# Kernel optimization log

Hardware: AMD Instinct MI355X
Metric: run time of the kernel (lower is better)

The kernel has to match this reference:

```python
import jax, jax.numpy as jnp
import numpy as np

B_, L_, V = 256, 256, 44
DM, DI, DS, DR, NL = 256, 512, 16, 16, 6  # d_model, d_inner, d_state, dt_rank, n_layers
MLP_H = 128


def setup_inputs():
    key = jax.random.key(0)
    ks = jax.random.split(key, 16)
    def nrm(i, shape, s=0.02):
        return jax.random.normal(ks[i], shape, jnp.float32) * s
    tok = jax.random.randint(ks[0], (B_, L_), 0, V, dtype=jnp.int32)
    mask = jax.random.randint(ks[1], (B_, L_), 0, 2, dtype=jnp.int32)
    emb = nrm(2, (V, 64), 0.02)
    emb = emb.at[0].set(0.0)  # padding_idx=0
    conv_w = nrm(3, (DM, 64, 3), 0.05)
    bn_gamma = jnp.ones((DM,), jnp.float32)
    bn_beta = jnp.zeros((DM,), jnp.float32)
    in_proj_w = nrm(4, (NL, 2 * DI, DM))
    conv1d_w = nrm(5, (NL, DI, 4), 0.2)
    conv1d_b = jnp.zeros((NL, DI), jnp.float32)
    x_proj_w = nrm(6, (NL, DR + 2 * DS, DI))
    dt_proj_w = nrm(7, (NL, DI, DR), 0.1)
    dt_proj_b = -4.0 + nrm(8, (NL, DI), 0.5)
    A_log = jnp.log(jnp.arange(1, DS + 1, dtype=jnp.float32))[None, None, :] * jnp.ones((NL, DI, 1), jnp.float32)
    Dp = jnp.ones((NL, DI), jnp.float32)
    out_proj_w = nrm(9, (NL, DM, DI))
    norm1_w = jnp.ones((NL, DM), jnp.float32)
    norm2_w = jnp.ones((NL, DM), jnp.float32)
    fc1_w = nrm(10, (NL, 2 * MLP_H, DM))
    fc2_w = nrm(11, (NL, DM, MLP_H))
    normf_w = jnp.ones((DM,), jnp.float32)
    normf_b = jnp.zeros((DM,), jnp.float32)
    bind_w = nrm(12, (3, DM))
    bind_b = jnp.zeros((3,), jnp.float32)
    return {"smiles_token_id": tok, "smiles_token_mask": mask, "emb": emb, "conv_w": conv_w,
            "bn_gamma": bn_gamma, "bn_beta": bn_beta, "in_proj_w": in_proj_w, "conv1d_w": conv1d_w,
            "conv1d_b": conv1d_b, "x_proj_w": x_proj_w, "dt_proj_w": dt_proj_w, "dt_proj_b": dt_proj_b,
            "A_log": A_log, "Dp": Dp, "out_proj_w": out_proj_w, "norm1_w": norm1_w, "norm2_w": norm2_w,
            "fc1_w": fc1_w, "fc2_w": fc2_w, "normf_w": normf_w, "normf_b": normf_b,
            "bind_w": bind_w, "bind_b": bind_b}


def rmsnorm(x, w, eps=1e-4):
    return x * jax.lax.rsqrt(jnp.mean(x * x, -1, keepdims=True) + eps) * w


def layernorm(x, w, b, eps=1e-4):
    mu = jnp.mean(x, -1, keepdims=True)
    var = jnp.mean((x - mu) ** 2, -1, keepdims=True)
    return (x - mu) * jax.lax.rsqrt(var + eps) * w + b


def mamba1(x, inw, cw, cb, xpw, dtw, dtb, Alog, D, outw):
    # x: [B,L,DM]
    B, L, _ = x.shape
    xz = x @ inw.T                                   # [B,L,2*DI]
    xi, z = jnp.split(xz, 2, axis=-1)
    # depthwise causal conv1d, kernel 4 (torch pads 3 then truncates to L)
    xp = jnp.pad(xi, ((0, 0), (3, 0), (0, 0)))
    xc = cb + sum(cw[:, k] * xp[:, k:k + L, :] for k in range(4))
    xc = jax.nn.silu(xc)                             # [B,L,DI]
    xdbl = xc @ xpw.T                                # [B,L,DR+2*DS]
    dt = xdbl[..., :DR]
    Bm = xdbl[..., DR:DR + DS]                       # [B,L,DS]
    Cm = xdbl[..., DR + DS:]
    dt = jax.nn.softplus(dt @ dtw.T + dtb)           # [B,L,DI]
    A = -jnp.exp(Alog)                               # [DI,DS]

    def step(h, inp):
        dt_t, u_t, B_t, C_t = inp                    # [B,DI],[B,DI],[B,DS],[B,DS]
        dA = jnp.exp(dt_t[:, :, None] * A)           # [B,DI,DS]
        h = dA * h + (dt_t * u_t)[:, :, None] * B_t[:, None, :]
        y = jnp.einsum('bdn,bn->bd', h, C_t)
        return h, y

    h0 = jnp.zeros((B, DI, DS), x.dtype)
    xs = (dt.transpose(1, 0, 2), xc.transpose(1, 0, 2), Bm.transpose(1, 0, 2), Cm.transpose(1, 0, 2))
    _, ys = jax.lax.scan(step, h0, xs)               # [L,B,DI]
    y = ys.transpose(1, 0, 2) + xc * D
    y = y * jax.nn.silu(z)
    return y @ outw.T                                # [B,L,DM]


def _forward(tok, mask, emb, conv_w, bn_gamma, bn_beta, in_proj_w, conv1d_w, conv1d_b,
             x_proj_w, dt_proj_w, dt_proj_b, A_log, Dp, out_proj_w, norm1_w, norm2_w,
             fc1_w, fc2_w, normf_w, normf_b, bind_w, bind_b):
    B, L = tok.shape
    x = emb[tok]                                     # [B,L,64]
    # conv embedding 64->256, k=3, pad=1 + BN(eval: mean 0, var 1, eps=1e-3) + relu
    xp = jnp.pad(x, ((0, 0), (1, 0 + 1), (0, 0)))
    y = sum(jnp.einsum('bli,oi->blo', xp[:, k:k + L, :], conv_w[:, :, k]) for k in range(3))
    y = y * (bn_gamma * jax.lax.rsqrt(jnp.float32(1.0 + 1e-3))) + bn_beta
    hidden = jax.nn.relu(y)                          # [B,L,DM]
    residual = None
    for i in range(NL):
        residual = hidden if residual is None else hidden + residual
        hs = rmsnorm(residual, norm1_w[i])
        hs = mamba1(hs, in_proj_w[i], conv1d_w[i], conv1d_b[i], x_proj_w[i],
                    dt_proj_w[i], dt_proj_b[i], A_log[i], Dp[i], out_proj_w[i])
        residual = hs + residual
        hs = rmsnorm(residual, norm2_w[i])
        yg = hs @ fc1_w[i].T                          # [B,L,2*MLP_H]
        y_, g = jnp.split(yg, 2, axis=-1)
        hidden = (y_ * jax.nn.silu(g)) @ fc2_w[i].T   # GatedMLP
        # dropout p=0.1 is identity in eval
    zf = layernorm(hidden + residual, normf_w, normf_b)
    m = mask[..., None].astype(jnp.float32)
    pool = (zf * m).sum(1) / m.sum(1)
    bind = pool @ bind_w.T + bind_b
    return jax.nn.sigmoid(bind)                       # [B,3]


def reference(smiles_token_id, smiles_token_mask, emb, conv_w, bn_gamma, bn_beta, in_proj_w,
              conv1d_w, conv1d_b, x_proj_w, dt_proj_w, dt_proj_b, A_log, Dp, out_proj_w,
              norm1_w, norm2_w, fc1_w, fc2_w, normf_w, normf_b, bind_w, bind_b):
    return _forward(smiles_token_id, smiles_token_mask, emb, conv_w, bn_gamma, bn_beta,
                    in_proj_w, conv1d_w, conv1d_b, x_proj_w, dt_proj_w, dt_proj_b, A_log, Dp,
                    out_proj_w, norm1_w, norm2_w, fc1_w, fc2_w, normf_w, normf_b, bind_w, bind_b)
```

## Files before the change

kernel.cpp:

```cpp
#include <hip/hip_runtime.h>
#include <math.h>

#define B_TOT 256
#define L_SEQ 256
#define DM 256
#define DI 512
#define DS 16
#define NL 6
#define MLPH 128
#define ED 64

typedef unsigned short u16;
typedef unsigned int   u32;
using bf16x8 = __attribute__((ext_vector_type(8))) short;
using f32x4  = __attribute__((ext_vector_type(4))) float;
using f32x2  = __attribute__((ext_vector_type(2))) float;

__device__ __forceinline__ float f_sigmoid(float x){ return 1.f/(1.f+__expf(-x)); }
__device__ __forceinline__ float f_silu(float x){ return x/(1.f+__expf(-x)); }
__device__ __forceinline__ u16 f2bf(float x){
  union { float f; u32 u; } v; v.f = x;
  u32 r = v.u + 0x7fffu + ((v.u >> 16) & 1u);
  return (u16)(r >> 16);
}
__device__ __forceinline__ float bf2f(u16 h){
  union { u32 u; float f; } v; v.u = ((u32)h) << 16; return v.f;
}
__device__ __forceinline__ f32x2 unpk2(u32 v){
  union { u32 u; float f; } a, b;
  a.u = (v & 0xffffu) << 16; b.u = v & 0xffff0000u;
  f32x2 r; r.x = a.f; r.y = b.f; return r;
}

__global__ __launch_bounds__(256) void k_cvt4(
    const float* __restrict__ s0, int n0, const float* __restrict__ s1, int n1,
    const float* __restrict__ s2, int n2, const float* __restrict__ s3, int n3,
    u16* __restrict__ d)
{
  int i = blockIdx.x*256 + threadIdx.x;
  float v;
  if (i < n0) v = s0[i];
  else if (i < n0+n1) v = s1[i-n0];
  else if (i < n0+n1+n2) v = s2[i-n0-n1];
  else if (i < n0+n1+n2+n3) v = s3[i-n0-n1-n2];
  else return;
  d[i] = f2bf(v);
}
__global__ __launch_bounds__(256) void k_cvt_xproj(const float* __restrict__ s, u16* __restrict__ d){
  int i = blockIdx.x*256 + threadIdx.x;
  int k = i & 511; int n = (i>>9) & 63; int l = i >> 15;
  d[i] = (n < 48) ? f2bf(s[((size_t)l*48 + n)*512 + k]) : (u16)0;
}

__global__ __launch_bounds__(256) void k_embed_conv(
    const int* __restrict__ tok, const float* __restrict__ emb,
    const float* __restrict__ cw, const float* __restrict__ gamma,
    const float* __restrict__ beta, u16* __restrict__ out)
{
  const int b  = blockIdx.y;
  const int lt = blockIdx.x;
  const int tid = threadIdx.x;
  __shared__ float xs[18][ED];
  for (int idx = tid; idx < 18*ED; idx += 256){
    int t = idx / ED, i = idx - t*ED;
    int l = lt*16 + t - 1;
    float v = 0.f;
    if (l >= 0 && l < L_SEQ) v = emb[tok[b*L_SEQ + l]*ED + i];
    xs[t][i] = v;
  }
  __syncthreads();
  const float g  = gamma[tid] * rsqrtf(1.001f);
  const float bt = beta[tid];
  const float* w = cw + (size_t)tid*(ED*3);
  float acc[16];
  #pragma unroll
  for (int t=0;t<16;t++) acc[t]=0.f;
  for (int i=0;i<ED;i++){
    float w0 = w[i*3+0], w1 = w[i*3+1], w2 = w[i*3+2];
    #pragma unroll
    for (int t=0;t<16;t++)
      acc[t] += xs[t][i]*w0 + xs[t+1][i]*w1 + xs[t+2][i]*w2;
  }
  #pragma unroll
  for (int t=0;t<16;t++){
    float v = acc[t]*g + bt;
    out[((size_t)(b*L_SEQ + lt*16 + t))*DM + tid] = f2bf(fmaxf(v, 0.f));
  }
}

__global__ __launch_bounds__(256) void k_rms_first(
    const u16* __restrict__ residual, const float* __restrict__ w, u16* __restrict__ out)
{
  const int row  = blockIdx.x*4 + (threadIdx.x >> 6);
  const int lane = threadIdx.x & 63;
  const size_t base = (size_t)row*DM;
  uint2 rv = *(const uint2*)(residual + base + lane*4);
  float v0 = bf2f((u16)(rv.x & 0xffff)), v1 = bf2f((u16)(rv.x >> 16));
  float v2 = bf2f((u16)(rv.y & 0xffff)), v3 = bf2f((u16)(rv.y >> 16));
  float ss = v0*v0 + v1*v1 + v2*v2 + v3*v3;
  #pragma unroll
  for (int m=1; m<64; m<<=1) ss += __shfl_xor(ss, m);
  const float sc = rsqrtf(ss*(1.f/DM) + 1e-4f);
  float4 wv = ((const float4*)w)[lane];
  u32 p0 = f2bf(v0*sc*wv.x) | ((u32)f2bf(v1*sc*wv.y) << 16);
  u32 p1 = f2bf(v2*sc*wv.z) | ((u32)f2bf(v3*sc*wv.w) << 16);
  uint2 pk; pk.x = p0; pk.y = p1;
  *(uint2*)(out + base + lane*4) = pk;
}

__global__ __launch_bounds__(256) void k_final_ln(
    const u16* __restrict__ x,
    const float* __restrict__ w, const float* __restrict__ bb, float* __restrict__ out)
{
  const int row  = blockIdx.x*4 + (threadIdx.x >> 6);
  const int lane = threadIdx.x & 63;
  const size_t base = (size_t)row*DM;
  uint2 rv = *(const uint2*)(x + base + lane*4);
  float4 v;
  v.x = bf2f((u16)(rv.x & 0xffff)); v.y = bf2f((u16)(rv.x >> 16));
  v.z = bf2f((u16)(rv.y & 0xffff)); v.w = bf2f((u16)(rv.y >> 16));
  float s = v.x + v.y + v.z + v.w;
  #pragma unroll
  for (int m=1; m<64; m<<=1) s += __shfl_xor(s, m);
  const float mu = s*(1.f/DM);
  float4 c; c.x=v.x-mu; c.y=v.y-mu; c.z=v.z-mu; c.w=v.w-mu;
  float ss = c.x*c.x + c.y*c.y + c.z*c.z + c.w*c.w;
  #pragma unroll
  for (int m=1; m<64; m<<=1) ss += __shfl_xor(ss, m);
  const float sc = rsqrtf(ss*(1.f/DM) + 1e-4f);
  float4 wv = ((const float4*)w)[lane];
  float4 bv = ((const float4*)bb)[lane];
  float4 o;
  o.x = c.x*sc*wv.x + bv.x; o.y = c.y*sc*wv.y + bv.y;
  o.z = c.z*sc*wv.z + bv.z; o.w = c.w*sc*wv.w + bv.w;
  ((float4*)(out + base))[lane] = o;
}

template<int BN, bool BF16OUT, bool SWIZ>
__global__ __launch_bounds__(256) void k_gemm_bf(
    const u16* __restrict__ A, const u16* __restrict__ W,
    void* __restrict__ Cv, int Nc, int K, int nmb)
{
  int bx, by;
  if (SWIZ){
    const int id = blockIdx.x;
    const int xcd = id & 7, rem = id >> 3;
    const int per = nmb >> 3;
    by = xcd*per + (rem % per);
    bx = rem / per;
  } else { bx = blockIdx.x; by = blockIdx.y; }
  const int n0 = bx * BN;
  const int m0 = by * 128;
  const int tid = threadIdx.x;
  const int w  = tid >> 6, l = tid & 63;
  const int wr = w >> 1, wc = w & 1;
  const int lr = l & 15, kb = l >> 4;
  constexpr int NJ = BN / 32;
  __shared__ uint4 As4[128*8];
  __shared__ uint4 Bs4[BN*8];
  f32x4 acc[4][NJ];
  #pragma unroll
  for (int i=0;i<4;i++)
    #pragma unroll
    for (int j=0;j<NJ;j++)
      acc[i][j] = (f32x4){0.f,0.f,0.f,0.f};
  const int srow = tid >> 3, schunk = tid & 7;
  for (int k0 = 0; k0 < K; k0 += 64){
    #pragma unroll
    for (int i=0;i<4;i++){
      int r = i*32 + srow;
      uint4 v = *(const uint4*)(A + (size_t)(m0 + r)*K + k0 + schunk*8);
      As4[r*8 + (schunk ^ (r & 7))] = v;
    }
    #pragma unroll
    for (int i=0;i<BN/32;i++){
      int r = i*32 + srow;
      uint4 v = *(const uint4*)(W + (size_t)(n0 + r)*K + k0 + schunk*8);
      Bs4[r*8 + (schunk ^ (r & 7))] = v;
    }
    __syncthreads();
    #pragma unroll
    for (int kk=0;kk<2;kk++){
      bf16x8 af[4], bfr[NJ];
      #pragma unroll
      for (int mi=0;mi<4;mi++){
        int r = wr*64 + mi*16 + lr;
        af[mi] = *(const bf16x8*)&As4[r*8 + ((kk*4 + kb) ^ (r & 7))];
      }
      #pragma unroll
      for (int ni=0;ni<NJ;ni++){
        int r = wc*(BN/2) + ni*16 + lr;
        bfr[ni] = *(const bf16x8*)&Bs4[r*8 + ((kk*4 + kb) ^ (r & 7))];
      }
      #pragma unroll
      for (int mi=0;mi<4;mi++)
        #pragma unroll
        for (int ni=0;ni<NJ;ni++)
          acc[mi][ni] = __builtin_amdgcn_mfma_f32_16x16x32_bf16(af[mi], bfr[ni], acc[mi][ni], 0, 0, 0);
    }
    __syncthreads();
  }
  #pragma unroll
  for (int mi=0;mi<4;mi++){
    #pragma unroll
    for (int ni=0;ni<NJ;ni++){
      int col = n0 + wc*(BN/2) + ni*16 + lr;
      if (col < Nc){
        #pragma unroll
        for (int r=0;r<4;r++){
          size_t row = (size_t)(m0 + wr*64 + mi*16 + kb*4 + r);
          if (BF16OUT) ((u16*)Cv)[row*Nc + col] = f2bf(acc[mi][ni][r]);
          else         ((float*)Cv)[row*Nc + col] = acc[mi][ni][r];
        }
      }
    }
  }
}

template<bool WRITE_HS>
__global__ __launch_bounds__(512) void k_gemm_rms(
    const u16* __restrict__ A, const u16* __restrict__ W,
    u16* __restrict__ residual, const float* __restrict__ nw,
    u16* __restrict__ hs, int K)
{
  const int m0 = blockIdx.x * 128;
  const int tid = threadIdx.x;
  const int w = tid >> 6, l = tid & 63;
  const int wr = w >> 1, wc = w & 1;
  const int lr = l & 15, kb = l >> 4;
  __shared__ uint4 As4[128*8];
  __shared__ uint4 Bs4[256*8];
  __shared__ float red[128][2];
  f32x4 acc[2][8];
  #pragma unroll
  for (int i=0;i<2;i++)
    #pragma unroll
    for (int j=0;j<8;j++) acc[i][j] = (f32x4){0.f,0.f,0.f,0.f};
  const int srow = tid >> 3, schunk = tid & 7;
  for (int k0 = 0; k0 < K; k0 += 64){
    #pragma unroll
    for (int i=0;i<2;i++){
      int r = i*64 + srow;
      uint4 v = *(const uint4*)(A + (size_t)(m0 + r)*K + k0 + schunk*8);
      As4[r*8 + (schunk ^ (r & 7))] = v;
    }
    #pragma unroll
    for (int i=0;i<4;i++){
      int r = i*64 + srow;
      uint4 v = *(const uint4*)(W + (size_t)r*K + k0 + schunk*8);
      Bs4[r*8 + (schunk ^ (r & 7))] = v;
    }
    __syncthreads();
    #pragma unroll
    for (int kk=0;kk<2;kk++){
      bf16x8 af[2], bfr[8];
      #pragma unroll
      for (int mi=0;mi<2;mi++){
        int r = wr*32 + mi*16 + lr;
        af[mi] = *(const bf16x8*)&As4[r*8 + ((kk*4 + kb) ^ (r & 7))];
      }
      #pragma unroll
      for (int ni=0;ni<8;ni++){
        int r = wc*128 + ni*16 + lr;
        bfr[ni] = *(const bf16x8*)&Bs4[r*8 + ((kk*4 + kb) ^ (r & 7))];
      }
      #pragma unroll
      for (int mi=0;mi<2;mi++)
        #pragma unroll
        for (int ni=0;ni<8;ni++)
          acc[mi][ni] = __builtin_amdgcn_mfma_f32_16x16x32_bf16(af[mi], bfr[ni], acc[mi][ni], 0, 0, 0);
    }
    __syncthreads();
  }
  float p[2][4];
  #pragma unroll
  for (int mi=0;mi<2;mi++)
    #pragma unroll
    for (int r=0;r<4;r++) p[mi][r] = 0.f;
  #pragma unroll
  for (int mi=0;mi<2;mi++){
    #pragma unroll
    for (int ni=0;ni<8;ni++){
      int col = wc*128 + ni*16 + lr;
      #pragma unroll
      for (int r=0;r<4;r++){
        int row = wr*32 + mi*16 + kb*4 + r;
        float v = acc[mi][ni][r] + bf2f(residual[(size_t)(m0+row)*DM + col]);
        acc[mi][ni][r] = v;
        p[mi][r] += v*v;
      }
    }
  }
  #pragma unroll
  for (int mi=0;mi<2;mi++)
    #pragma unroll
    for (int r=0;r<4;r++){
      float s = p[mi][r];
      s += __shfl_xor(s, 1); s += __shfl_xor(s, 2);
      s += __shfl_xor(s, 4); s += __shfl_xor(s, 8);
      p[mi][r] = s;
    }
  if (lr == 0){
    #pragma unroll
    for (int mi=0;mi<2;mi++)
      #pragma unroll
      for (int r=0;r<4;r++)
        red[wr*32 + mi*16 + kb*4 + r][wc] = p[mi][r];
  }
  __syncthreads();
  #pragma unroll
  for (int mi=0;mi<2;mi++){
    float scm[4];
    #pragma unroll
    for (int r=0;r<4;r++){
      int row = wr*32 + mi*16 + kb*4 + r;
      scm[r] = rsqrtf((red[row][0]+red[row][1])*(1.f/DM) + 1e-4f);
    }
    #pragma unroll
    for (int ni=0;ni<8;ni++){
      int col = wc*128 + ni*16 + lr;
      float wn = WRITE_HS ? nw[col] : 0.f;
      #pragma unroll
      for (int r=0;r<4;r++){
        int row = wr*32 + mi*16 + kb*4 + r;
        float v = acc[mi][ni][r];
        residual[(size_t)(m0+row)*DM + col] = f2bf(v);
        if (WRITE_HS) hs[(size_t)(m0+row)*DM + col] = f2bf(v*scm[r]*wn);
      }
    }
  }
}

__global__ __launch_bounds__(512) void k_fc1_glu(
    const u16* __restrict__ A, const u16* __restrict__ W, u16* __restrict__ out)
{
  const int K = DM;
  const int m0 = blockIdx.x * 128;
  const int tid = threadIdx.x;
  const int w = tid >> 6, l = tid & 63;
  const int wr = w >> 1, wc = w & 1;
  const int lr = l & 15, kb = l >> 4;
  __shared__ uint4 As4[128*8];
  __shared__ uint4 Bs4[256*8];
  f32x4 acc[2][8];
  #pragma unroll
  for (int i=0;i<2;i++)
    #pragma unroll
    for (int j=0;j<8;j++) acc[i][j] = (f32x4){0.f,0.f,0.f,0.f};
  const int srow = tid >> 3, schunk = tid & 7;
  for (int k0 = 0; k0 < K; k0 += 64){
    #pragma unroll
    for (int i=0;i<2;i++){
      int r = i*64 + srow;
      uint4 v = *(const uint4*)(A + (size_t)(m0 + r)*K + k0 + schunk*8);
      As4[r*8 + (schunk ^ (r & 7))] = v;
    }
    #pragma unroll
    for (int i=0;i<4;i++){
      int r = i*64 + srow;
      uint4 v = *(const uint4*)(W + (size_t)r*K + k0 + schunk*8);
      Bs4[r*8 + (schunk ^ (r & 7))] = v;
    }
    __syncthreads();
    #pragma unroll
    for (int kk=0;kk<2;kk++){
      bf16x8 af[2], bfr[8];
      #pragma unroll
      for (int mi=0;mi<2;mi++){
        int r = wr*32 + mi*16 + lr;
        af[mi] = *(const bf16x8*)&As4[r*8 + ((kk*4 + kb) ^ (r & 7))];
      }
      #pragma unroll
      for (int ni=0;ni<8;ni++){
        int r = (ni < 4) ? (wc*64 + ni*16 + lr) : (128 + wc*64 + (ni-4)*16 + lr);
        bfr[ni] = *(const bf16x8*)&Bs4[r*8 + ((kk*4 + kb) ^ (r & 7))];
      }
      #pragma unroll
      for (int mi=0;mi<2;mi++)
        #pragma unroll
        for (int ni=0;ni<8;ni++)
          acc[mi][ni] = __builtin_amdgcn_mfma_f32_16x16x32_bf16(af[mi], bfr[ni], acc[mi][ni], 0, 0, 0);
    }
    __syncthreads();
  }
  #pragma unroll
  for (int mi=0;mi<2;mi++){
    #pragma unroll
    for (int ni=0;ni<4;ni++){
      int jcol = wc*64 + ni*16 + lr;
      #pragma unroll
      for (int r=0;r<4;r++){
        int row = wr*32 + mi*16 + kb*4 + r;
        float y = acc[mi][ni][r];
        float g = acc[mi][ni+4][r];
        out[(size_t)(m0+row)*MLPH + jcol] = f2bf(y * f_silu(g));
      }
    }
  }
}

__global__ __launch_bounds__(256) void k_conv1d_silu(
    const u16* __restrict__ xz, const float* __restrict__ cw,
    const float* __restrict__ cb, u16* __restrict__ xcb)
{
  const int idx = blockIdx.x*256 + threadIdx.x;
  const int d0 = (idx & 63) * 8;
  const int m  = idx >> 6;
  const int l  = m & (L_SEQ-1);
  float acc[8];
  #pragma unroll
  for (int j=0;j<8;j++) acc[j] = cb[d0+j];
  float4 wv[8];
  #pragma unroll
  for (int j=0;j<8;j++) wv[j] = *(const float4*)(cw + (d0+j)*4);
  #pragma unroll
  for (int t=0;t<4;t++){
    if (l >= 3-t){
      bf16x8 v = *(const bf16x8*)(xz + (size_t)(m-3+t)*1024 + d0);
      #pragma unroll
      for (int j=0;j<8;j++){
        float wj = (t==0)?wv[j].x:(t==1)?wv[j].y:(t==2)?wv[j].z:wv[j].w;
        acc[j] += wj * bf2f((u16)v[j]);
      }
    }
  }
  u16 o[8];
  #pragma unroll
  for (int j=0;j<8;j++) o[j] = f2bf(f_silu(acc[j]));
  *(uint4*)(xcb + (size_t)m*DI + d0) = *(uint4*)o;
}

__global__ __launch_bounds__(512) void k_scan6(
    const float* __restrict__ xdbl, const u16* __restrict__ xcb,
    const u16* __restrict__ xz, u16* __restrict__ ybf,
    const float* __restrict__ A_log, const float* __restrict__ Dp,
    const float* __restrict__ dtw, const float* __restrict__ dtb)
{
  const int b = blockIdx.x;
  const int lane = threadIdx.x & 63;
  const int w = threadIdx.x >> 6;
  const int d = blockIdx.y*64 + lane;
  __shared__ __align__(16) float BD[L_SEQ][48];
  __shared__ u32 HT2[8][8][64];
  __shared__ float SD[8][64];
  const size_t rowbase = (size_t)b*L_SEQ;
  {
    const float4* src = (const float4*)(xdbl + rowbase*48);
    float4* dst = (float4*)&BD[0][0];
    #pragma unroll
    for (int j=0;j<6;j++) dst[threadIdx.x + j*512] = src[threadIdx.x + j*512];
  }
  f32x2 w2[8];
  #pragma unroll
  for (int k=0;k<8;k++){
    w2[k].x = dtw[(size_t)d*16 + 2*k];
    w2[k].y = dtw[(size_t)d*16 + 2*k + 1];
  }
  const float dtb_r = dtb[d];
  bool structured = true;
  #pragma unroll
  for (int n=0;n<16;n++){
    float Ar = -__expf(A_log[(size_t)d*16 + n]);
    structured = structured && (fabsf(Ar + (float)(n+1)) < 1e-4f*(float)(n+1));
  }
  const float Dv = Dp[d];
  const int l0 = w*32;
  float u_cur[8], z_cur[8];
  #pragma unroll
  for (int s=0;s<8;s++){
    u_cur[s] = bf2f(xcb[(rowbase+l0+s)*DI + d]);
    z_cur[s] = bf2f(xz [(rowbase+l0+s)*1024 + 512 + d]);
  }
  __syncthreads();
  f32x2 h2[8];
  #pragma unroll
  for (int i=0;i<8;i++) h2[i] = (f32x2){0.f,0.f};
  float cum = 0.f;
  #pragma unroll
  for (int t8=0; t8<4; ++t8){
    float u_nxt[8], z_nxt[8];
    if (t8 < 3){
      #pragma unroll
      for (int s=0;s<8;s++){
        u_nxt[s] = bf2f(xcb[(rowbase+l0+t8*8+8+s)*DI + d]);
        z_nxt[s] = bf2f(xz [(rowbase+l0+t8*8+8+s)*1024 + 512 + d]);
      }
    }
    #pragma unroll
    for (int s=0;s<8;s++){
      const int l = l0 + t8*8 + s;
      const float u_v = u_cur[s], z_v = z_cur[s];
      const float4* bd4 = (const float4*)&BD[l][0];
      float4 X[4], Bq[4], Cq[4];
      #pragma unroll
      for (int j=0;j<4;j++){ X[j]=bd4[j]; Bq[j]=bd4[4+j]; Cq[j]=bd4[8+j]; }
      f32x2 xp[8], bp[8], cp[8];
      #pragma unroll
      for (int j=0;j<4;j++){
        xp[2*j]   = (f32x2){X[j].x,  X[j].y};  xp[2*j+1] = (f32x2){X[j].z,  X[j].w};
        bp[2*j]   = (f32x2){Bq[j].x, Bq[j].y}; bp[2*j+1] = (f32x2){Bq[j].z, Bq[j].w};
        cp[2*j]   = (f32x2){Cq[j].x, Cq[j].y}; cp[2*j+1] = (f32x2){Cq[j].z, Cq[j].w};
      }
      f32x2 a2 = xp[0]*w2[0], a2b = xp[1]*w2[1];
      #pragma unroll
      for (int j=2;j<8;j+=2){ a2 += xp[j]*w2[j]; a2b += xp[j+1]*w2[j+1]; }
      const float xr = dtb_r + (a2.x + a2.y) + (a2b.x + a2b.y);
      const float ex = __expf(xr);
      const float dt_v = (xr > 20.f) ? xr : __logf(1.f + ex);
      cum += dt_v;
      const f32x2 dtu2 = (f32x2){dt_v*u_v, dt_v*u_v};
      f32x2 y2 = (f32x2){0.f,0.f}, y2b = (f32x2){0.f,0.f};
      if (structured){
        const float p = 1.f/(1.f + ex);
        f32x2 pw = (f32x2){p, p*p};
        const f32x2 e2 = (f32x2){pw.y, pw.y};
        #pragma unroll
        for (int i=0;i<8;i++){
          h2[i] = pw*h2[i] + dtu2*bp[i];
          if (i&1) y2b += h2[i]*cp[i]; else y2 += h2[i]*cp[i];
          if (i<7) pw = pw*e2;
        }
      } else {
        #pragma unroll
        for (int i=0;i<8;i++){
          float Ar0 = -__expf(A_log[(size_t)d*16 + 2*i]);
          float Ar1 = -__expf(A_log[(size_t)d*16 + 2*i+1]);
          f32x2 dA = (f32x2){__expf(dt_v*Ar0), __expf(dt_v*Ar1)};
          h2[i] = dA*h2[i] + dtu2*bp[i];
          if (i&1) y2b += h2[i]*cp[i]; else y2 += h2[i]*cp[i];
        }
      }
      const float y = (y2.x + y2.y) + (y2b.x + y2b.y);
      const float sz = f_silu(z_v);
      ybf[(rowbase+l)*DI + d] = f2bf((y + u_v*Dv) * sz);
    }
    if (t8 < 3){
      #pragma unroll
      for (int s=0;s<8;s++){ u_cur[s]=u_nxt[s]; z_cur[s]=z_nxt[s]; }
    }
  }
  SD[w][lane] = cum;
  #pragma unroll
  for (int i=0;i<8;i++)
    HT2[w][i][lane] = (u32)f2bf(h2[i].x) | ((u32)f2bf(h2[i].y) << 16);
  __syncthreads();
  if (w == 0) return;
  f32x2 H02[8];
  #pragma unroll
  for (int i=0;i<8;i++) H02[i] = (f32x2){0.f,0.f};
  for (int c=0; c<w; ++c){
    float sdt = SD[c][lane];
    if (structured){
      float q = __expf(-sdt);
      f32x2 qw = (f32x2){q, q*q};
      const f32x2 e2 = (f32x2){qw.y, qw.y};
      #pragma unroll
      for (int i=0;i<8;i++){
        H02[i] = H02[i]*qw + unpk2(HT2[c][i][lane]);
        if (i<7) qw = qw*e2;
      }
    } else {
      #pragma unroll
      for (int i=0;i<8;i++){
        float Ar0 = -__expf(A_log[(size_t)d*16 + 2*i]);
        float Ar1 = -__expf(A_log[(size_t)d*16 + 2*i+1]);
        f32x2 dA = (f32x2){__expf(Ar0*sdt), __expf(Ar1*sdt)};
        H02[i] = H02[i]*dA + unpk2(HT2[c][i][lane]);
      }
    }
  }
  float q = 1.f;
  float cum2 = 0.f;
  #pragma unroll
  for (int s=0;s<8;s++)
    z_cur[s] = bf2f(xz[(rowbase+l0+s)*1024 + 512 + d]);
  #pragma unroll
  for (int t8=0; t8<4; ++t8){
    float z_nxt[8];
    if (t8 < 3){
      #pragma unroll
      for (int s=0;s<8;s++)
        z_nxt[s] = bf2f(xz[(rowbase+l0+t8*8+8+s)*1024 + 512 + d]);
    }
    #pragma unroll
    for (int s=0;s<8;s++){
      const int l = l0 + t8*8 + s;
      const float4* bd4 = (const float4*)&BD[l][0];
      float4 X[4], Cq[4];
      #pragma unroll
      for (int j=0;j<4;j++){ X[j]=bd4[j]; Cq[j]=bd4[8+j]; }
      f32x2 xp[8], cp[8];
      #pragma unroll
      for (int j=0;j<4;j++){
        xp[2*j]   = (f32x2){X[j].x,  X[j].y};  xp[2*j+1] = (f32x2){X[j].z,  X[j].w};
        cp[2*j]   = (f32x2){Cq[j].x, Cq[j].y}; cp[2*j+1] = (f32x2){Cq[j].z, Cq[j].w};
      }
      f32x2 a2 = xp[0]*w2[0], a2b = xp[1]*w2[1];
      #pragma unroll
      for (int j=2;j<8;j+=2){ a2 += xp[j]*w2[j]; a2b += xp[j+1]*w2[j+1]; }
      const float xr = dtb_r + (a2.x + a2.y) + (a2b.x + a2b.y);
      const float ex = __expf(xr);
      f32x2 cacc = (f32x2){0.f,0.f}, caccb = (f32x2){0.f,0.f};
      if (structured){
        const float p = 1.f/(1.f + ex);
        q *= p;
        f32x2 qw = (f32x2){q, q*q};
        const f32x2 e2 = (f32x2){qw.y, qw.y};
        #pragma unroll
        for (int i=0;i<8;i++){
          f32x2 t = (cp[i]*H02[i])*qw;
          if (i&1) caccb += t; else cacc += t;
          if (i<7) qw = qw*e2;
        }
      } else {
        const float dt_v = (xr > 20.f) ? xr : __logf(1.f + ex);
        cum2 += dt_v;
        #pragma unroll
        for (int i=0;i<8;i++){
          float Ar0 = -__expf(A_log[(size_t)d*16 + 2*i]);
          float Ar1 = -__expf(A_log[(size_t)d*16 + 2*i+1]);
          f32x2 dA = (f32x2){__expf(Ar0*cum2), __expf(Ar1*cum2)};
          f32x2 t = (cp[i]*H02[i])*dA;
          if (i&1) caccb += t; else cacc += t;
        }
      }
      const float corr = (cacc.x + cacc.y) + (caccb.x + caccb.y);
      const float sz = f_silu(z_cur[s]);
      const size_t off = (rowbase+l)*DI + d;
      float prev = bf2f(ybf[off]);
      ybf[off] = f2bf(prev + corr*sz);
    }
    if (t8 < 3){
      #pragma unroll
      for (int s=0;s<8;s++) z_cur[s] = z_nxt[s];
    }
  }
}

__global__ __launch_bounds__(1024) void k_pool(
    const float* __restrict__ zf, const int* __restrict__ mask,
    float* __restrict__ pool, int b0)
{
  const int b = blockIdx.x;
  const int d = threadIdx.x & 255;
  const int lg = threadIdx.x >> 8;
  __shared__ float red[4][DM];
  __shared__ float msum[4];
  float s = 0.f, ms = 0.f;
  for (int l = lg*64; l < lg*64 + 64; ++l){
    float mv = (float)mask[(size_t)(b0+b)*L_SEQ + l];
    s  += mv * zf[((size_t)b*L_SEQ + l)*DM + d];
    ms += mv;
  }
  red[lg][d] = s;
  if (d == 0) msum[lg] = ms;
  __syncthreads();
  if (lg == 0){
    float tot = red[0][d] + red[1][d] + red[2][d] + red[3][d];
    float m = msum[0] + msum[1] + msum[2] + msum[3];
    pool[(size_t)(b0+b)*DM + d] = tot/m;
  }
}

__global__ __launch_bounds__(64) void k_bind(
    const float* __restrict__ pool, const float* __restrict__ bw,
    const float* __restrict__ bb, float* __restrict__ out)
{
  const int b = blockIdx.x;
  const int lane = threadIdx.x;
  float4 p = ((const float4*)(pool + (size_t)b*DM))[lane];
  #pragma unroll
  for (int j=0;j<3;j++){
    float4 w = ((const float4*)(bw + (size_t)j*DM))[lane];
    float s = p.x*w.x + p.y*w.y + p.z*w.z + p.w*w.w;
    #pragma unroll
    for (int m=1;m<64;m<<=1) s += __shfl_xor(s, m);
    if (lane==0) out[b*3 + j] = f_sigmoid(s + bb[j]);
  }
}

extern "C" void kernel_launch(void* const* d_in, const int* in_sizes, int n_in,
                              void* d_out, int out_size, void* d_ws, size_t ws_size,
                              hipStream_t stream)
{
  const int*   tok       = (const int*)  d_in[0];
  const int*   mask      = (const int*)  d_in[1];
  const float* emb       = (const float*)d_in[2];
  const float* conv_w    = (const float*)d_in[3];
  const float* bn_gamma  = (const float*)d_in[4];
  const float* bn_beta   = (const float*)d_in[5];
  const float* in_proj_w = (const float*)d_in[6];
  const float* conv1d_w  = (const float*)d_in[7];
  const float* conv1d_b  = (const float*)d_in[8];
  const float* x_proj_w  = (const float*)d_in[9];
  const float* dt_proj_w = (const float*)d_in[10];
  const float* dt_proj_b = (const float*)d_in[11];
  const float* A_log     = (const float*)d_in[12];
  const float* Dp        = (const float*)d_in[13];
  const float* out_proj_w= (const float*)d_in[14];
  const float* norm1_w   = (const float*)d_in[15];
  const float* norm2_w   = (const float*)d_in[16];
  const float* fc1_w     = (const float*)d_in[17];
  const float* fc2_w     = (const float*)d_in[18];
  const float* normf_w   = (const float*)d_in[19];
  const float* normf_b   = (const float*)d_in[20];
  const float* bind_w    = (const float*)d_in[21];
  const float* bind_b    = (const float*)d_in[22];
  float* outp = (float*)d_out;

  char* base = (char*)d_ws;
  size_t off = 0;
  const int NIN = NL*2*DI*DM, NOUT = NL*DM*DI, NF1 = NL*2*MLPH*DM, NF2 = NL*DM*MLPH, NXP = NL*64*DI;
  u16* w_in  = (u16*)(base + off); off += (size_t)NIN*2;
  u16* w_out = (u16*)(base + off); off += (size_t)NOUT*2;
  u16* w_f1  = (u16*)(base + off); off += (size_t)NF1*2;
  u16* w_f2  = (u16*)(base + off); off += (size_t)NF2*2;
  u16* w_xp  = (u16*)(base + off); off += (size_t)NXP*2;
  float* pool = (float*)(base + off); off += (size_t)B_TOT*DM*4;
  const size_t fixed = off;

  const size_t perRow = 48*4 + (256+1024+512+512+256+128)*2;
  int Bc = B_TOT;
  while (Bc > 1 && fixed + (size_t)Bc*L_SEQ*perRow > ws_size) Bc >>= 1;
  const int Mc = Bc * L_SEQ;

  u16*   residual = (u16*)(base + off);   off += (size_t)Mc*DM*2;
  float* xdbl     = (float*)(base + off); off += (size_t)Mc*48*4;
  u16*   xz       = (u16*)(base + off);   off += (size_t)Mc*1024*2;
  u16*   xcb      = (u16*)(base + off);   off += (size_t)Mc*DI*2;
  u16*   ybf      = (u16*)(base + off);   off += (size_t)Mc*DI*2;
  u16*   hsbf     = (u16*)(base + off);   off += (size_t)Mc*DM*2;
  u16*   glubf    = (u16*)(base + off);   off += (size_t)Mc*MLPH*2;
  float* zf       = (float*)xz;

  const int NCVT = NIN + NOUT + NF1 + NF2;
  k_cvt4<<<(NCVT+255)/256, 256, 0, stream>>>(in_proj_w, NIN, out_proj_w, NOUT,
                                             fc1_w, NF1, fc2_w, NF2, w_in);
  k_cvt_xproj<<<(NXP+255)/256, 256, 0, stream>>>(x_proj_w, w_xp);

  const int nmb = Mc/128;
  const bool canSwiz = (nmb & 7) == 0;
  const int nchunks = B_TOT / Bc;
  for (int c = 0; c < nchunks; ++c){
    const int b0 = c * Bc;
    k_embed_conv<<<dim3(L_SEQ/16, Bc), 256, 0, stream>>>(
        tok + (size_t)b0*L_SEQ, emb, conv_w, bn_gamma, bn_beta, residual);
    k_rms_first<<<Mc/4, 256, 0, stream>>>(residual, norm1_w, hsbf);

    for (int i = 0; i < NL; ++i){
      const u16*  inw  = w_in  + (size_t)i*(2*DI)*DM;
      const float* cw  = conv1d_w  + (size_t)i*DI*4;
      const float* cb  = conv1d_b  + (size_t)i*DI;
      const u16*  xpw  = w_xp  + (size_t)i*64*DI;
      const float* dtw = dt_proj_w + (size_t)i*DI*16;
      const float* dtb = dt_proj_b + (size_t)i*DI;
      const float* Alg = A_log     + (size_t)i*DI*DS;
      const float* Dpt = Dp        + (size_t)i*DI;
      const u16*  outw = w_out + (size_t)i*DM*DI;
      const float* n2w = norm2_w   + (size_t)i*DM;
      const u16*  f1w  = w_f1  + (size_t)i*(2*MLPH)*DM;
      const u16*  f2w  = w_f2  + (size_t)i*DM*MLPH;

      if (canSwiz)
        k_gemm_bf<128,true,true ><<<dim3(8*nmb), 256, 0, stream>>>(hsbf, inw, xz, 2*DI, DM, nmb);
      else
        k_gemm_bf<128,true,false><<<dim3(8, nmb), 256, 0, stream>>>(hsbf, inw, xz, 2*DI, DM, nmb);
      k_conv1d_silu<<<(Mc*64)/256, 256, 0, stream>>>(xz, cw, cb, xcb);
      k_gemm_bf<64, false,false><<<dim3(1, nmb), 256, 0, stream>>>(xcb, xpw, xdbl, 48, DI, nmb);
      k_scan6<<<dim3(Bc, 8), 512, 0, stream>>>(xdbl, xcb, xz, ybf, Alg, Dpt, dtw, dtb);
      k_gemm_rms<true><<<Mc/128, 512, 0, stream>>>(ybf, outw, residual, n2w, hsbf, DI);
      k_fc1_glu<<<Mc/128, 512, 0, stream>>>(hsbf, f1w, glubf);
      if (i < NL-1)
        k_gemm_rms<true ><<<Mc/128, 512, 0, stream>>>(glubf, f2w, residual,
                                                      norm1_w + (size_t)(i+1)*DM, hsbf, MLPH);
      else
        k_gemm_rms<false><<<Mc/128, 512, 0, stream>>>(glubf, f2w, residual,
                                                      nullptr, nullptr, MLPH);
    }

    k_final_ln<<<Mc/4, 256, 0, stream>>>(residual, normf_w, normf_b, zf);
    k_pool<<<Bc, 1024, 0, stream>>>(zf, mask, pool, b0);
  }
  k_bind<<<B_TOT, 64, 0, stream>>>(pool, bind_w, bind_b, outp);
}
```

Measured before the change: 3.658 ms.

## Precompute dt projection in separate kernel and stream it into scan

```diff
diff --git a/kernel.cpp b/kernel.cpp
--- a/kernel.cpp
+++ b/kernel.cpp
@@ -430,17 +430,41 @@
   *(uint4*)(xcb + (size_t)m*DI + d0) = *(uint4*)o;
 }
 
-__global__ __launch_bounds__(512) void k_scan6(
+__global__ __launch_bounds__(256) void k_dtraw(
+    const float* __restrict__ xdbl, const float* __restrict__ dtw,
+    const float* __restrict__ dtb, u16* __restrict__ dtraw)
+{
+  const int idx = blockIdx.x*256 + threadIdx.x;
+  const int d = idx & (DI-1);
+  const int m0 = (idx >> 9) * 8;
+  const float* w = dtw + (size_t)d*16;
+  float4 w0 = *(const float4*)(w),   w1 = *(const float4*)(w+4),
+         w2 = *(const float4*)(w+8), w3 = *(const float4*)(w+12);
+  const float b = dtb[d];
+  #pragma unroll
+  for (int i=0;i<8;i++){
+    const float4* xr = (const float4*)(xdbl + (size_t)(m0+i)*48);
+    float4 x0 = xr[0], x1 = xr[1], x2 = xr[2], x3 = xr[3];
+    float a = b
+      + x0.x*w0.x + x0.y*w0.y + x0.z*w0.z + x0.w*w0.w
+      + x1.x*w1.x + x1.y*w1.y + x1.z*w1.z + x1.w*w1.w
+      + x2.x*w2.x + x2.y*w2.y + x2.z*w2.z + x2.w*w2.w
+      + x3.x*w3.x + x3.y*w3.y + x3.z*w3.z + x3.w*w3.w;
+    dtraw[(size_t)(m0+i)*DI + d] = f2bf(a);
+  }
+}
+
+__global__ __launch_bounds__(512) void k_scan8(
     const float* __restrict__ xdbl, const u16* __restrict__ xcb,
-    const u16* __restrict__ xz, u16* __restrict__ ybf,
-    const float* __restrict__ A_log, const float* __restrict__ Dp,
-    const float* __restrict__ dtw, const float* __restrict__ dtb)
+    const u16* __restrict__ xz, const u16* __restrict__ dtraw,
+    u16* __restrict__ ybf,
+    const float* __restrict__ A_log, const float* __restrict__ Dp)
 {
   const int b = blockIdx.x;
   const int lane = threadIdx.x & 63;
   const int w = threadIdx.x >> 6;
   const int d = blockIdx.y*64 + lane;
-  __shared__ __align__(16) float BD[L_SEQ][48];
+  __shared__ __align__(16) float BD[L_SEQ][32];
   __shared__ u32 HT2[8][8][64];
   __shared__ float SD[8][64];
   const size_t rowbase = (size_t)b*L_SEQ;
@@ -448,15 +472,12 @@
     const float4* src = (const float4*)(xdbl + rowbase*48);
     float4* dst = (float4*)&BD[0][0];
     #pragma unroll
-    for (int j=0;j<6;j++) dst[threadIdx.x + j*512] = src[threadIdx.x + j*512];
-  }
-  f32x2 w2[8];
-  #pragma unroll
-  for (int k=0;k<8;k++){
-    w2[k].x = dtw[(size_t)d*16 + 2*k];
-    w2[k].y = dtw[(size_t)d*16 + 2*k + 1];
-  }
-  const float dtb_r = dtb[d];
+    for (int j=0;j<4;j++){
+      int t = threadIdx.x + j*512;
+      int r = t >> 3, c = t & 7;
+      dst[t] = src[r*12 + 4 + c];
+    }
+  }
   bool structured = true;
   #pragma unroll
   for (int n=0;n<16;n++){
@@ -465,11 +486,12 @@
   }
   const float Dv = Dp[d];
   const int l0 = w*32;
-  float u_cur[8], z_cur[8];
+  float u_cur[8], z_cur[8], t_cur[8];
   #pragma unroll
   for (int s=0;s<8;s++){
-    u_cur[s] = bf2f(xcb[(rowbase+l0+s)*DI + d]);
-    z_cur[s] = bf2f(xz [(rowbase+l0+s)*1024 + 512 + d]);
+    u_cur[s] = bf2f(xcb  [(rowbase+l0+s)*DI + d]);
+    z_cur[s] = bf2f(xz   [(rowbase+l0+s)*1024 + 512 + d]);
+    t_cur[s] = bf2f(dtraw[(rowbase+l0+s)*DI + d]);
   }
   __syncthreads();
   f32x2 h2[8];
@@ -478,33 +500,29 @@
   float cum = 0.f;
   #pragma unroll
   for (int t8=0; t8<4; ++t8){
-    float u_nxt[8], z_nxt[8];
+    float u_nxt[8], z_nxt[8], t_nxt[8];
     if (t8 < 3){
       #pragma unroll
       for (int s=0;s<8;s++){
-        u_nxt[s] = bf2f(xcb[(rowbase+l0+t8*8+8+s)*DI + d]);
-        z_nxt[s] = bf2f(xz [(rowbase+l0+t8*8+8+s)*1024 + 512 + d]);
+        u_nxt[s] = bf2f(xcb  [(rowbase+l0+t8*8+8+s)*DI + d]);
+        z_nxt[s] = bf2f(xz   [(rowbase+l0+t8*8+8+s)*1024 + 512 + d]);
+        t_nxt[s] = bf2f(dtraw[(rowbase+l0+t8*8+8+s)*DI + d]);
       }
     }
     #pragma unroll
     for (int s=0;s<8;s++){
       const int l = l0 + t8*8 + s;
-      const float u_v = u_cur[s], z_v = z_cur[s];
+      const float u_v = u_cur[s], z_v = z_cur[s], xr = t_cur[s];
       const float4* bd4 = (const float4*)&BD[l][0];
-      float4 X[4], Bq[4], Cq[4];
-      #pragma unroll
-      for (int j=0;j<4;j++){ X[j]=bd4[j]; Bq[j]=bd4[4+j]; Cq[j]=bd4[8+j]; }
-      f32x2 xp[8], bp[8], cp[8];
+      float4 Bq[4], Cq[4];
+      #pragma unroll
+      for (int j=0;j<4;j++){ Bq[j]=bd4[j]; Cq[j]=bd4[4+j]; }
+      f32x2 bp[8], cp[8];
       #pragma unroll
       for (int j=0;j<4;j++){
-        xp[2*j]   = (f32x2){X[j].x,  X[j].y};  xp[2*j+1] = (f32x2){X[j].z,  X[j].w};
         bp[2*j]   = (f32x2){Bq[j].x, Bq[j].y}; bp[2*j+1] = (f32x2){Bq[j].z, Bq[j].w};
         cp[2*j]   = (f32x2){Cq[j].x, Cq[j].y}; cp[2*j+1] = (f32x2){Cq[j].z, Cq[j].w};
       }
-      f32x2 a2 = xp[0]*w2[0], a2b = xp[1]*w2[1];
-      #pragma unroll
-      for (int j=2;j<8;j+=2){ a2 += xp[j]*w2[j]; a2b += xp[j+1]*w2[j+1]; }
-      const float xr = dtb_r + (a2.x + a2.y) + (a2b.x + a2b.y);
       const float ex = __expf(xr);
       const float dt_v = (xr > 20.f) ? xr : __logf(1.f + ex);
       cum += dt_v;
@@ -536,7 +554,7 @@
     }
     if (t8 < 3){
       #pragma unroll
-      for (int s=0;s<8;s++){ u_cur[s]=u_nxt[s]; z_cur[s]=z_nxt[s]; }
+      for (int s=0;s<8;s++){ u_cur[s]=u_nxt[s]; z_cur[s]=z_nxt[s]; t_cur[s]=t_nxt[s]; }
     }
   }
   SD[w][lane] = cum;
@@ -572,33 +590,33 @@
   float q = 1.f;
   float cum2 = 0.f;
   #pragma unroll
-  for (int s=0;s<8;s++)
-    z_cur[s] = bf2f(xz[(rowbase+l0+s)*1024 + 512 + d]);
+  for (int s=0;s<8;s++){
+    z_cur[s] = bf2f(xz   [(rowbase+l0+s)*1024 + 512 + d]);
+    t_cur[s] = bf2f(dtraw[(rowbase+l0+s)*DI + d]);
+  }
   #pragma unroll
   for (int t8=0; t8<4; ++t8){
-    float z_nxt[8];
+    float z_nxt[8], t_nxt[8];
     if (t8 < 3){
       #pragma unroll
-      for (int s=0;s<8;s++)
-        z_nxt[s] = bf2f(xz[(rowbase+l0+t8*8+8+s)*1024 + 512 + d]);
+      for (int s=0;s<8;s++){
+        z_nxt[s] = bf2f(xz   [(rowbase+l0+t8*8+8+s)*1024 + 512 + d]);
+        t_nxt[s] = bf2f(dtraw[(rowbase+l0+t8*8+8+s)*DI + d]);
+      }
     }
     #pragma unroll
     for (int s=0;s<8;s++){
       const int l = l0 + t8*8 + s;
+      const float xr = t_cur[s];
       const float4* bd4 = (const float4*)&BD[l][0];
-      float4 X[4], Cq[4];
-      #pragma unroll
-      for (int j=0;j<4;j++){ X[j]=bd4[j]; Cq[j]=bd4[8+j]; }
-      f32x2 xp[8], cp[8];
+      float4 Cq[4];
+      #pragma unroll
+      for (int j=0;j<4;j++) Cq[j] = bd4[4+j];
+      f32x2 cp[8];
       #pragma unroll
       for (int j=0;j<4;j++){
-        xp[2*j]   = (f32x2){X[j].x,  X[j].y};  xp[2*j+1] = (f32x2){X[j].z,  X[j].w};
         cp[2*j]   = (f32x2){Cq[j].x, Cq[j].y}; cp[2*j+1] = (f32x2){Cq[j].z, Cq[j].w};
       }
-      f32x2 a2 = xp[0]*w2[0], a2b = xp[1]*w2[1];
-      #pragma unroll
-      for (int j=2;j<8;j+=2){ a2 += xp[j]*w2[j]; a2b += xp[j+1]*w2[j+1]; }
-      const float xr = dtb_r + (a2.x + a2.y) + (a2b.x + a2b.y);
       const float ex = __expf(xr);
       f32x2 cacc = (f32x2){0.f,0.f}, caccb = (f32x2){0.f,0.f};
       if (structured){
@@ -632,7 +650,7 @@
     }
     if (t8 < 3){
       #pragma unroll
-      for (int s=0;s<8;s++) z_cur[s] = z_nxt[s];
+      for (int s=0;s<8;s++){ z_cur[s] = z_nxt[s]; t_cur[s] = t_nxt[s]; }
     }
   }
 }
@@ -719,7 +737,7 @@
   float* pool = (float*)(base + off); off += (size_t)B_TOT*DM*4;
   const size_t fixed = off;
 
-  const size_t perRow = 48*4 + (256+1024+512+512+256+128)*2;
+  const size_t perRow = 48*4 + (256+1024+512+512+512+256+128)*2;
   int Bc = B_TOT;
   while (Bc > 1 && fixed + (size_t)Bc*L_SEQ*perRow > ws_size) Bc >>= 1;
   const int Mc = Bc * L_SEQ;
@@ -728,6 +746,7 @@
   float* xdbl     = (float*)(base + off); off += (size_t)Mc*48*4;
   u16*   xz       = (u16*)(base + off);   off += (size_t)Mc*1024*2;
   u16*   xcb      = (u16*)(base + off);   off += (size_t)Mc*DI*2;
+  u16*   dtraw    = (u16*)(base + off);   off += (size_t)Mc*DI*2;
   u16*   ybf      = (u16*)(base + off);   off += (size_t)Mc*DI*2;
   u16*   hsbf     = (u16*)(base + off);   off += (size_t)Mc*DM*2;
   u16*   glubf    = (u16*)(base + off);   off += (size_t)Mc*MLPH*2;
@@ -767,7 +786,8 @@
         k_gemm_bf<128,true,false><<<dim3(8, nmb), 256, 0, stream>>>(hsbf, inw, xz, 2*DI, DM, nmb);
       k_conv1d_silu<<<(Mc*64)/256, 256, 0, stream>>>(xz, cw, cb, xcb);
       k_gemm_bf<64, false,false><<<dim3(1, nmb), 256, 0, stream>>>(xcb, xpw, xdbl, 48, DI, nmb);
-      k_scan6<<<dim3(Bc, 8), 512, 0, stream>>>(xdbl, xcb, xz, ybf, Alg, Dpt, dtw, dtb);
+      k_dtraw<<<(Mc/8)*DI/256, 256, 0, stream>>>(xdbl, dtw, dtb, dtraw);
+      k_scan8<<<dim3(Bc, 8), 512, 0, stream>>>(xdbl, xcb, xz, dtraw, ybf, Alg, Dpt);
       k_gemm_rms<true><<<Mc/128, 512, 0, stream>>>(ybf, outw, residual, n2w, hsbf, DI);
       k_fc1_glu<<<Mc/128, 512, 0, stream>>>(hsbf, f1w, glubf);
       if (i < NL-1)
```

After: 4.881 ms. 33.4% more time.
